# Kernel optimization log

Measured on AMD Instinct MI355X. Metric: run time of the kernel, lower is better.

## Reference

```python
import jax, jax.numpy as jnp
import numpy as np


def _ste(q, x):
    # straight-through estimator: forward = q, gradient = identity w.r.t. x
    return x + jax.lax.stop_gradient(q - x)


def quant_w(w, bit_w=8):
    # symmetric per-tensor weight quantization fused into QConv2d
    qmax = 2.0 ** (bit_w - 1) - 1.0
    scale = jnp.max(jnp.abs(w)) / qmax
    q = jnp.clip(jnp.round(w / scale), -qmax, qmax) * scale
    return _ste(q, w)


def quant_a(x, bit_a=8):
    # unsigned activation quantizer: clamp to [0,1], uniform bit_a levels
    n = 2.0 ** bit_a - 1.0
    xc = jnp.clip(x, 0.0, 1.0)
    q = jnp.round(xc * n) / n
    return _ste(q, xc)


def exp_norm2d(x, gamma, beta, eps=1e-5):
    # instance-style norm: per (N, C) statistics over spatial dims, affine
    mean = jnp.mean(x, axis=(2, 3), keepdims=True)
    var = jnp.var(x, axis=(2, 3), keepdims=True)
    xn = (x - mean) * jax.lax.rsqrt(var + eps)
    return xn * gamma[None, :, None, None] + beta[None, :, None, None]


def qconv(x, w, stride, pad, bit_w=8):
    wq = quant_w(w, bit_w)
    return jax.lax.conv_general_dilated(
        x, wq, window_strides=(stride, stride),
        padding=[(pad, pad), (pad, pad)],
        dimension_numbers=('NCHW', 'OIHW', 'NCHW'))


def setup_inputs() -> dict:
    key = jax.random.key(0)
    ks = jax.random.split(key, 4)
    C_in, C_out, H = 256, 512, 56
    return {
        'x': jax.random.normal(ks[0], (32, C_in, H, H), jnp.float32),
        'w1': jax.random.normal(ks[1], (C_out, C_in, 3, 3), jnp.float32) * 0.05,
        'g1': jnp.ones((C_out,), jnp.float32),
        'b1': jnp.zeros((C_out,), jnp.float32),
        'w2': jax.random.normal(ks[2], (C_out, C_out, 3, 3), jnp.float32) * 0.05,
        'g2': jnp.ones((C_out,), jnp.float32),
        'b2': jnp.zeros((C_out,), jnp.float32),
        'wp': jax.random.normal(ks[3], (C_out, C_in, 1, 1), jnp.float32) * 0.05,
        'gp': jnp.ones((C_out,), jnp.float32),
        'bp': jnp.zeros((C_out,), jnp.float32),
    }


def reference(x, w1, g1, b1, w2, g2, b2, wp, gp, bp):
    # main branch: QConv(s2) -> ExpNorm -> act quant -> QConv(s1) -> ExpNorm
    h = qconv(x, w1, stride=2, pad=1)
    h = exp_norm2d(h, g1, b1)
    h = quant_a(h, bit_a=8)
    h = qconv(h, w2, stride=1, pad=1)
    h = exp_norm2d(h, g2, b2)
    # projection shortcut: QConv 1x1 stride 2 -> ExpNorm
    s = qconv(x, wp, stride=2, pad=0)
    s = exp_norm2d(s, gp, bp)
    return h + s
```

## Files before the change

kernel.cpp:

```cpp
#include <hip/hip_runtime.h>
#include <cstdint>
#include <cstddef>


typedef unsigned short ushort_t;
typedef __attribute__((ext_vector_type(8))) short bf16x8;
typedef __attribute__((ext_vector_type(4))) int i32x4;

#define NB   32
#define C_IN 256
#define HIN  56
#define CO   512
#define OHW  784
#define OWD  28
#define MTOT (NB * OHW)

#define S_X  (6.0f / 127.0f)

constexpr size_t OFF_XH   = 0;
constexpr size_t OFF_A1   = OFF_XH  + 25690112;
constexpr size_t OFF_H2   = OFF_A1  + 12845056;
constexpr size_t OFF_S    = OFF_H2  + 25690112;
constexpr size_t OFF_WT1  = OFF_S   + 25690112;
constexpr size_t OFF_WT2  = OFF_WT1 + 1179648;
constexpr size_t OFF_WTP  = OFF_WT2 + 2359296;
constexpr size_t OFF_A1N  = OFF_WTP + 131072;
constexpr size_t OFF_B1N  = OFF_A1N + 65536;
constexpr size_t OFF_A2N  = OFF_B1N + 65536;
constexpr size_t OFF_B2N  = OFF_A2N + 65536;
constexpr size_t OFF_APN  = OFF_B2N + 65536;
constexpr size_t OFF_BPN  = OFF_APN + 65536;
constexpr size_t OFF_MX   = OFF_BPN + 65536;
constexpr size_t OFF_ZB   = OFF_MX  + 16;
constexpr size_t OFF_CS   = OFF_ZB  + 2048;
constexpr size_t OFF_PSUM = OFF_CS  + 18432;
constexpr size_t ZERO_LEN = 16 + 2048 + 18432 + 393216;

__device__ __forceinline__ ushort_t f2bf(float f) {
    unsigned u = __float_as_uint(f);
    u += 0x7FFFu + ((u >> 16) & 1u);
    return (ushort_t)(u >> 16);
}
__device__ __forceinline__ float bf2f(ushort_t u) {
    return __uint_as_float(((unsigned)u) << 16);
}

__device__ __forceinline__ void async_copy16(const void* g, const void* l) {
    auto gp = (const __attribute__((address_space(1))) unsigned int*)(uintptr_t)g;
    auto lp = (__attribute__((address_space(3))) unsigned int*)(unsigned int)(uintptr_t)l;
    __builtin_amdgcn_global_load_lds(gp, lp, 16, 0, 0);
}

__global__ void to_nhwc_i8_k(const float* __restrict__ x, signed char* __restrict__ xh) {
    __shared__ float tile[64][33];
    const int wt0 = blockIdx.x * 32;
    const int ct0 = blockIdx.y * 64;
    const int nh  = blockIdx.z;
    const int n = nh / HIN, h = nh - n * HIN;
    {
        const int tx = threadIdx.x & 31;
        const int ty = threadIdx.x >> 5;
        const int w  = wt0 + tx;
#pragma unroll
        for (int j = 0; j < 8; ++j) {
            int cl = ty + j * 8;
            if (w < HIN)
                tile[cl][tx] = x[(((size_t)n * C_IN + ct0 + cl) * HIN + h) * HIN + w];
        }
    }
    __syncthreads();
    {
        const float inv = 127.0f / 6.0f;
        const int tc4 = threadIdx.x & 15;
        const int tw  = threadIdx.x >> 4;
#pragma unroll
        for (int j = 0; j < 2; ++j) {
            int wl = tw + j * 16;
            int w  = wt0 + wl;
            if (w < HIN) {
                unsigned pk = 0;
#pragma unroll
                for (int k = 0; k < 4; ++k) {
                    float v = tile[tc4 * 4 + k][wl];
                    float q = fminf(127.f, fmaxf(-127.f, rintf(v * inv)));
                    pk |= ((unsigned)((int)q & 0xFF)) << (8 * k);
                }
                *(unsigned*)&xh[(((size_t)n * HIN + h) * HIN + w) * C_IN + ct0 + tc4 * 4] = pk;
            }
        }
    }
}

__global__ void absmax3_k(const float* __restrict__ w1, int n1,
                          const float* __restrict__ w2, int n2,
                          const float* __restrict__ wp, int np,
                          unsigned* out) {
    const float4* w; int nelem;
    if (blockIdx.y == 0)      { w = (const float4*)w1; nelem = n1 >> 2; }
    else if (blockIdx.y == 1) { w = (const float4*)w2; nelem = n2 >> 2; }
    else                      { w = (const float4*)wp; nelem = np >> 2; }
    int stride = gridDim.x * blockDim.x;
    float m = 0.f;
    for (int i = blockIdx.x * blockDim.x + threadIdx.x; i < nelem; i += stride) {
        float4 v = w[i];
        m = fmaxf(m, fmaxf(fmaxf(fabsf(v.x), fabsf(v.y)),
                           fmaxf(fabsf(v.z), fabsf(v.w))));
    }
#pragma unroll
    for (int off = 32; off > 0; off >>= 1)
        m = fmaxf(m, __shfl_down(m, off));
    if ((threadIdx.x & 63) == 0) atomicMax(out + blockIdx.y, __float_as_uint(m));
}

__global__ void quantw_all_k(const float* __restrict__ w1,
                             const float* __restrict__ w2,
                             const float* __restrict__ wp,
                             const unsigned* __restrict__ mx,
                             signed char* __restrict__ wt1,
                             signed char* __restrict__ wt2,
                             signed char* __restrict__ wtp,
                             float* __restrict__ cs) {
    const int b = blockIdx.x;
    if (b < 4608) {
        int idx = b * 256 + threadIdx.x;
        float scale = __uint_as_float(mx[0]) * (1.0f / 127.0f);
        float inv   = scale > 0.f ? 1.0f / scale : 0.f;
        int khw = idx / (CO * C_IN);
        int r   = idx - khw * (CO * C_IN);
        int co  = r / C_IN;
        int ci  = r - co * C_IN;
        float v  = w1[((size_t)co * C_IN + ci) * 9 + khw];
        float qv = rintf(v * inv);
        qv = fminf(127.f, fmaxf(-127.f, qv));
        wt1[idx] = (signed char)(int)qv;
    } else if (b < 13824) {
        int idx = (b - 4608) * 256 + threadIdx.x;
        float scale = __uint_as_float(mx[1]) * (1.0f / 127.0f);
        float inv   = scale > 0.f ? 1.0f / scale : 0.f;
        int khw = idx / (CO * CO);
        int r   = idx - khw * (CO * CO);
        int co  = r / CO;
        int ci  = r - co * CO;
        float v  = w2[((size_t)co * CO + ci) * 9 + khw];
        float qv = rintf(v * inv);
        qv = fminf(127.f, fmaxf(-127.f, qv));
        int iq = (int)qv;
        wt2[idx] = (signed char)iq;
        int s = iq;
#pragma unroll
        for (int off = 32; off > 0; off >>= 1)
            s += __shfl_down(s, off);
        if ((threadIdx.x & 63) == 0) atomicAdd(&cs[khw * CO + co], (float)s);
    } else {
        int idx = (b - 13824) * 256 + threadIdx.x;
        float scale = __uint_as_float(mx[2]) * (1.0f / 127.0f);
        float inv   = scale > 0.f ? 1.0f / scale : 0.f;
        int co  = idx / C_IN;
        int ci  = idx - co * C_IN;
        float v  = wp[(size_t)co * C_IN + ci];
        float qv = rintf(v * inv);
        qv = fminf(127.f, fmaxf(-127.f, qv));
        wtp[idx] = (signed char)(int)qv;
    }
}

template <int CIN, int KH, int KW, int STRIDE, int PAD, int IH, int IW, bool OFFSET>
__launch_bounds__(1024, 4)
__global__ void conv_i8_t(const signed char* __restrict__ xin,
                          const signed char* __restrict__ wt,
                          const float* __restrict__ colsum,
                          const unsigned* __restrict__ mxw,
                          float sxa,
                          ushort_t* __restrict__ out,
                          const signed char* __restrict__ zbuf,
                          float* __restrict__ psum, float* __restrict__ pss) {
    constexpr int BK   = 64;
    constexpr int CKT  = CIN / BK;
    constexpr int KT   = KH * KW * CKT;
    constexpr int NPER = KT / 2;

    __shared__ alignas(16) signed char As[4 * 256 * BK];
    __shared__ alignas(16) signed char Bs[4 * 256 * BK];

    const int tid  = threadIdx.x;
    const int lane = tid & 63;
    const int wv   = tid >> 6;
    const int wm   = wv >> 2;
    const int wn   = wv & 3;
    const int lrow = lane & 15;
    const int lq   = lane >> 4;

    const int bid = blockIdx.x;
    const int xcd = bid & 7;
    const int j   = bid >> 3;
    const int wg  = (xcd < 4 ? xcd * 25 : 100 + (xcd - 4) * 24) + j;
    const int m0  = (wg >> 1) * 256;
    const int co0 = (wg & 1) * 256;

    const int arow = tid >> 2;
    const int ach  = tid & 3;
    int abase; unsigned amask; int bco;
    {
        int m   = m0 + arow;
        int n   = m / OHW;
        int sp  = m - n * OHW;
        int oh  = sp / OWD, ow = sp - oh * OWD;
        int ihb = oh * STRIDE - PAD, iwb = ow * STRIDE - PAD;
        int swz = (ach ^ ((arow >> 1) & 3)) * 16;
        abase = (n * (IH * IW) + ihb * IW + iwb) * CIN + swz;
        unsigned mk = 0;
#pragma unroll
        for (int kh = 0; kh < KH; ++kh)
#pragma unroll
            for (int kw = 0; kw < KW; ++kw) {
                int ih = ihb + kh, iw = iwb + kw;
                if ((unsigned)ih < (unsigned)IH && (unsigned)iw < (unsigned)IW)
                    mk |= 1u << (kh * KW + kw);
            }
        amask = mk;
        bco = (co0 + arow) * CIN + swz;
    }

    auto stageA = [&](int buf, int aoff, int khw) {
        const signed char* src = ((amask >> khw) & 1)
            ? xin + (abase + aoff) : zbuf;
        async_copy16(src, (const void*)&As[buf * 16384 + wv * 1024]);
    };
    auto stageB = [&](int buf, int boff) {
        async_copy16(wt + (boff + bco), (const void*)&Bs[buf * 16384 + wv * 1024]);
    };

    i32x4 acc[4][4];
#pragma unroll
    for (int a = 0; a < 4; ++a)
#pragma unroll
        for (int b = 0; b < 4; ++b) acc[a][b] = {0, 0, 0, 0};

    stageB(0, 0);  stageA(0, 0, 0);
    stageB(1, BK); stageA(1, BK, 0);
    asm volatile("s_waitcnt vmcnt(0)" ::: "memory");
    __builtin_amdgcn_s_barrier();

    int khw_n = 0, kw_n = 0, ck_n = 2;
    int aoff_n = 2 * BK;
    int boff_n = 2 * BK;

#pragma unroll 1
    for (int p = 0; p < NPER; ++p) {
        const int t0 = 2 * p;
        if (p + 1 < NPER) {
#pragma unroll
            for (int u = 0; u < 2; ++u) {
                const int buf = (t0 + 2 + u) & 3;
                stageB(buf, boff_n);
                stageA(buf, aoff_n, khw_n);
                ck_n++;
                if (ck_n == CKT) {
                    ck_n = 0; khw_n++; kw_n++;
                    if (kw_n == KW) { kw_n = 0; aoff_n += (IW - KW) * CIN + BK; }
                    else            { aoff_n += BK; }
                    boff_n += (CO - 1) * CIN + BK;
                } else {
                    aoff_n += BK; boff_n += BK;
                }
            }
        }
        __builtin_amdgcn_sched_barrier(0);

#pragma unroll
        for (int sub = 0; sub < 2; ++sub) {
            const signed char* Acur = &As[((t0 + sub) & 3) * 16384];
            const signed char* Bcur = &Bs[((t0 + sub) & 3) * 16384];
            i32x4 af[4], bfr[4];
#pragma unroll
            for (int mi = 0; mi < 4; ++mi) {
                const int row = wm * 64 + mi * 16 + lrow;
                af[mi] = *(const i32x4*)&Acur[row * BK + ((lq ^ ((row >> 1) & 3)) * 16)];
            }
#pragma unroll
            for (int ni = 0; ni < 4; ++ni) {
                const int row = wn * 64 + ni * 16 + lrow;
                bfr[ni] = *(const i32x4*)&Bcur[row * BK + ((lq ^ ((row >> 1) & 3)) * 16)];
            }
#pragma unroll
            for (int mi = 0; mi < 4; ++mi)
#pragma unroll
                for (int ni = 0; ni < 4; ++ni)
                    acc[mi][ni] = __builtin_amdgcn_mfma_i32_16x16x64_i8(
                        af[mi], bfr[ni], acc[mi][ni], 0, 0, 0);
        }

        asm volatile("s_waitcnt vmcnt(0)" ::: "memory");
        __builtin_amdgcn_sched_barrier(0);
        __builtin_amdgcn_s_barrier();
    }

    const int mb = m0 + wm * 64 + lq * 4;
    const int cb = co0 + wn * 64 + lrow;
    const float sw = __uint_as_float(*mxw) * (1.0f / 127.0f);
    float sc, c128 = 0.f;
    if constexpr (OFFSET) { sc = sw * (1.0f / 255.0f); c128 = 128.0f * sc; }
    else                  { sc = sxa * sw; }

    float Sall[4], Sr0[4], Sr2[4], Sc0[4], Sc2[4], K0[4], K2[4], K6[4], K8[4];
    if constexpr (OFFSET) {
#pragma unroll
        for (int ni = 0; ni < 4; ++ni) {
            float cs9[9];
#pragma unroll
            for (int k = 0; k < 9; ++k) cs9[k] = colsum[k * CO + cb + ni * 16];
            Sall[ni] = cs9[0]+cs9[1]+cs9[2]+cs9[3]+cs9[4]+cs9[5]+cs9[6]+cs9[7]+cs9[8];
            Sr0[ni] = cs9[0]+cs9[1]+cs9[2];  Sr2[ni] = cs9[6]+cs9[7]+cs9[8];
            Sc0[ni] = cs9[0]+cs9[3]+cs9[6];  Sc2[ni] = cs9[2]+cs9[5]+cs9[8];
            K0[ni] = cs9[0]; K2[ni] = cs9[2]; K6[ni] = cs9[6]; K8[ni] = cs9[8];
        }
    }

    const int n0 = m0 / OHW;
    const int mS = (n0 + 1) * OHW;
    float sv[2][4], qvv[2][4];
#pragma unroll
    for (int g = 0; g < 2; ++g)
#pragma unroll
        for (int ni = 0; ni < 4; ++ni) { sv[g][ni] = 0.f; qvv[g][ni] = 0.f; }

#pragma unroll
    for (int mi = 0; mi < 4; ++mi)
#pragma unroll
        for (int r = 0; r < 4; ++r) {
            const int m  = mb + mi * 16 + r;
            const int n  = m / OHW;
            const int sp = m - n * OHW;
            const int oh = sp / OWD, ow = sp - oh * OWD;
            const int g  = (m >= mS) ? 1 : 0;
#pragma unroll
            for (int ni = 0; ni < 4; ++ni) {
                float val;
                if constexpr (OFFSET) {
                    float T = Sall[ni];
                    if (oh == 0)       T -= Sr0[ni];
                    if (oh == OWD - 1) T -= Sr2[ni];
                    if (ow == 0)       T -= Sc0[ni];
                    if (ow == OWD - 1) T -= Sc2[ni];
                    if (oh == 0 && ow == 0)             T += K0[ni];
                    if (oh == 0 && ow == OWD - 1)       T += K2[ni];
                    if (oh == OWD - 1 && ow == 0)       T += K6[ni];
                    if (oh == OWD - 1 && ow == OWD - 1) T += K8[ni];
                    val = sc * (float)acc[mi][ni][r] + c128 * T;
                } else {
                    val = sc * (float)acc[mi][ni][r];
                }
                out[(size_t)m * CO + (cb + ni * 16)] = f2bf(val);
                sv[g][ni] += val; qvv[g][ni] += val * val;
            }
        }
#pragma unroll
    for (int d = 16; d <= 32; d <<= 1)
#pragma unroll
        for (int g = 0; g < 2; ++g)
#pragma unroll
            for (int ni = 0; ni < 4; ++ni) {
                sv[g][ni]  += __shfl_xor(sv[g][ni], d);
                qvv[g][ni] += __shfl_xor(qvv[g][ni], d);
            }
    if (lq == 0) {
        const bool split = (mS < m0 + 256);
#pragma unroll
        for (int ni = 0; ni < 4; ++ni) {
            atomicAdd(&psum[n0 * CO + cb + ni * 16], sv[0][ni]);
            atomicAdd(&pss [n0 * CO + cb + ni * 16], qvv[0][ni]);
            if (split) {
                atomicAdd(&psum[(n0 + 1) * CO + cb + ni * 16], sv[1][ni]);
                atomicAdd(&pss [(n0 + 1) * CO + cb + ni * 16], qvv[1][ni]);
            }
        }
    }
}

__global__ void statsf3_k(const float* __restrict__ ps0, const float* __restrict__ qs0,
                          const float* __restrict__ g0, const float* __restrict__ bb0,
                          float* __restrict__ ao0, float* __restrict__ bo0,
                          const float* __restrict__ ps1, const float* __restrict__ qs1,
                          const float* __restrict__ g1, const float* __restrict__ bb1,
                          float* __restrict__ ao1, float* __restrict__ bo1,
                          const float* __restrict__ ps2, const float* __restrict__ qs2,
                          const float* __restrict__ g2, const float* __restrict__ bb2,
                          float* __restrict__ ao2, float* __restrict__ bo2) {
    const float *ps, *qs, *g, *bb; float *ao, *bo;
    if (blockIdx.y == 0)      { ps = ps0; qs = qs0; g = g0; bb = bb0; ao = ao0; bo = bo0; }
    else if (blockIdx.y == 1) { ps = ps1; qs = qs1; g = g1; bb = bb1; ao = ao1; bo = bo1; }
    else                      { ps = ps2; qs = qs2; g = g2; bb = bb2; ao = ao2; bo = bo2; }
    int idx = blockIdx.x * 256 + threadIdx.x;
    int c = idx & 511;
    float s  = ps[idx];
    float ss = qs[idx];
    float mean = s * (1.0f / 784.0f);
    float var  = ss * (1.0f / 784.0f) - mean * mean;
    float rstd = rsqrtf(var + 1e-5f);
    float a = rstd * g[c];
    ao[idx] = a;
    bo[idx] = bb[c] - mean * a;
}

__global__ void norm_quant_i8_k(const ushort_t* __restrict__ h, const float* __restrict__ a_,
                                const float* __restrict__ b_, signed char* __restrict__ o) {
    int idx = blockIdx.x * 256 + threadIdx.x;
    int row = idx >> 6;
    int c0  = (idx & 63) * 8;
    int n   = row / OHW;
    bf16x8 v = ((const bf16x8*)h)[idx];
    const float* ap = a_ + n * CO + c0;
    const float* bp = b_ + n * CO + c0;
    unsigned lo = 0, hi = 0;
#pragma unroll
    for (int k = 0; k < 8; ++k) {
        float f = bf2f((ushort_t)v[k]) * ap[k] + bp[k];
        float kq = rintf(fminf(fmaxf(f, 0.f), 1.f) * 255.f);
        int s8 = (int)kq - 128;
        unsigned b = (unsigned)(s8 & 0xFF);
        if (k < 4) lo |= b << (8 * k);
        else       hi |= b << (8 * (k - 4));
    }
    ((uint2*)o)[idx] = make_uint2(lo, hi);
}

__global__ void final_k(const ushort_t* __restrict__ h2, const ushort_t* __restrict__ s,
                        const float* __restrict__ a2, const float* __restrict__ b2,
                        const float* __restrict__ ap_, const float* __restrict__ bp_,
                        float* __restrict__ out) {
    __shared__ float tile[64][33];
    const int sp0 = blockIdx.x * 32;
    const int c0  = blockIdx.y * 64;
    const int n   = blockIdx.z;
    const int tx  = threadIdx.x & 31;
    const int ty  = threadIdx.x >> 5;
#pragma unroll
    for (int j = 0; j < 4; ++j) {
        int spl = ty + j * 8;
        int sp  = sp0 + spl;
        if (sp < OHW) {
            int c = c0 + tx * 2;
            size_t ix = ((size_t)n * OHW + sp) * CO + c;
            int ci = n * CO + c;
            ushort2 vh = *(const ushort2*)&h2[ix];
            ushort2 vs = *(const ushort2*)&s[ix];
            tile[tx * 2][spl] =
                bf2f(vh.x) * a2[ci] + b2[ci] + bf2f(vs.x) * ap_[ci] + bp_[ci];
            tile[tx * 2 + 1][spl] =
                bf2f(vh.y) * a2[ci + 1] + b2[ci + 1] + bf2f(vs.y) * ap_[ci + 1] + bp_[ci + 1];
        }
    }
    __syncthreads();
    const int sp = sp0 + tx;
#pragma unroll
    for (int j = 0; j < 8; ++j) {
        int cl = ty + j * 8;
        if (sp < OHW)
            out[((size_t)n * CO + c0 + cl) * OHW + sp] = tile[cl][tx];
    }
}

extern "C" void kernel_launch(void* const* d_in, const int* in_sizes, int n_in,
                              void* d_out, int out_size, void* d_ws, size_t ws_size,
                              hipStream_t stream) {
    const float* x  = (const float*)d_in[0];
    const float* w1 = (const float*)d_in[1];
    const float* g1 = (const float*)d_in[2];
    const float* b1 = (const float*)d_in[3];
    const float* w2 = (const float*)d_in[4];
    const float* g2 = (const float*)d_in[5];
    const float* b2 = (const float*)d_in[6];
    const float* wp = (const float*)d_in[7];
    const float* gp = (const float*)d_in[8];
    const float* bp = (const float*)d_in[9];
    float* out = (float*)d_out;
    char* ws = (char*)d_ws;

    signed char* xh    = (signed char*)(ws + OFF_XH);
    signed char* a1    = (signed char*)(ws + OFF_A1);
    ushort_t*    h2    = (ushort_t*)(ws + OFF_H2);
    ushort_t*    sbuf  = (ushort_t*)(ws + OFF_S);
    signed char* wt1i  = (signed char*)(ws + OFF_WT1);
    signed char* wt2i  = (signed char*)(ws + OFF_WT2);
    signed char* wtpi  = (signed char*)(ws + OFF_WTP);
    float*    a1n  = (float*)(ws + OFF_A1N);
    float*    b1n  = (float*)(ws + OFF_B1N);
    float*    a2n  = (float*)(ws + OFF_A2N);
    float*    b2n  = (float*)(ws + OFF_B2N);
    float*    apn  = (float*)(ws + OFF_APN);
    float*    bpn  = (float*)(ws + OFF_BPN);
    unsigned* mx   = (unsigned*)(ws + OFF_MX);
    signed char* zb = (signed char*)(ws + OFF_ZB);
    float*    cs   = (float*)(ws + OFF_CS);
    float*    psum1 = (float*)(ws + OFF_PSUM);
    float*    pss1  = (float*)(ws + OFF_PSUM + 65536);
    float*    psum2 = (float*)(ws + OFF_PSUM + 131072);
    float*    pss2  = (float*)(ws + OFF_PSUM + 196608);
    float*    psump = (float*)(ws + OFF_PSUM + 262144);
    float*    pssp  = (float*)(ws + OFF_PSUM + 327680);
    ushort_t* h1   = (ushort_t*)out;

    hipMemsetAsync(ws + OFF_MX, 0, ZERO_LEN, stream);

    to_nhwc_i8_k<<<dim3(2, 4, NB * HIN), 256, 0, stream>>>(x, xh);
    absmax3_k<<<dim3(512, 3), 256, 0, stream>>>(w1, CO * C_IN * 9,
                                                w2, CO * CO * 9,
                                                wp, C_IN * CO, mx);
    quantw_all_k<<<dim3(14336), 256, 0, stream>>>(w1, w2, wp, mx,
                                                  wt1i, wt2i, wtpi, cs);

    conv_i8_t<C_IN, 3, 3, 2, 1, HIN, HIN, false>
        <<<dim3(196), 1024, 0, stream>>>(xh, wt1i, cs, mx + 0, S_X, h1, zb,
                                         psum1, pss1);
    statsf3_k<<<dim3(64, 1), 256, 0, stream>>>(psum1, pss1, g1, b1, a1n, b1n,
                                               psum1, pss1, g1, b1, a1n, b1n,
                                               psum1, pss1, g1, b1, a1n, b1n);
    norm_quant_i8_k<<<dim3(MTOT * CO / 8 / 256), 256, 0, stream>>>(h1, a1n, b1n, a1);

    conv_i8_t<CO, 3, 3, 1, 1, 28, 28, true>
        <<<dim3(196), 1024, 0, stream>>>(a1, wt2i, cs, mx + 1, 1.0f, h2, zb,
                                         psum2, pss2);
    conv_i8_t<C_IN, 1, 1, 2, 0, HIN, HIN, false>
        <<<dim3(196), 1024, 0, stream>>>(xh, wtpi, cs, mx + 2, S_X, sbuf, zb,
                                         psump, pssp);

    statsf3_k<<<dim3(64, 2), 256, 0, stream>>>(psum2, pss2, g2, b2, a2n, b2n,
                                               psump, pssp, gp, bp, apn, bpn,
                                               psum2, pss2, g2, b2, a2n, b2n);

    final_k<<<dim3(25, 8, NB), 256, 0, stream>>>(h2, sbuf, a2n, b2n, apn, bpn, out);
}
```

Measured before the change: 277.4 us.

## Pre-swizzle weights into MFMA fragment layout and load B directly from global

Weight quantization now writes int8 weights in a per-k-tile, per-16-row fragment layout matching the MFMA operand order. The conv kernel drops the B shared-memory buffers and async B staging, and each lane loads its B fragments straight from global (L2-resident) memory at the start of each iteration. This halves LDS use and removes LDS traffic for B. The cost is global-load latency exposed in the inner loop, since B is no longer prefetched ahead, and redundant B loads across the wm warps.

```diff
diff --git a/kernel.cpp b/kernel.cpp
--- a/kernel.cpp
+++ b/kernel.cpp
@@ -49,6 +49,11 @@
     auto gp = (const __attribute__((address_space(1))) unsigned int*)(uintptr_t)g;
     auto lp = (__attribute__((address_space(3))) unsigned int*)(unsigned int)(uintptr_t)l;
     __builtin_amdgcn_global_load_lds(gp, lp, 16, 0, 0);
+}
+
+__device__ __forceinline__ size_t wfrag_addr(int kt, int co, int ci) {
+    return (size_t)kt * 32768 + (size_t)(co >> 4) * 1024 +
+           (size_t)(((co & 15) | (((ci >> 4) & 3) << 4)) * 16 + (ci & 15));
 }
 
 __global__ void to_nhwc_i8_k(const float* __restrict__ x, signed char* __restrict__ xh) {
@@ -132,7 +137,7 @@
         float v  = w1[((size_t)co * C_IN + ci) * 9 + khw];
         float qv = rintf(v * inv);
         qv = fminf(127.f, fmaxf(-127.f, qv));
-        wt1[idx] = (signed char)(int)qv;
+        wt1[wfrag_addr(khw * 4 + (ci >> 6), co, ci)] = (signed char)(int)qv;
     } else if (b < 13824) {
         int idx = (b - 4608) * 256 + threadIdx.x;
         float scale = __uint_as_float(mx[1]) * (1.0f / 127.0f);
@@ -145,7 +150,7 @@
         float qv = rintf(v * inv);
         qv = fminf(127.f, fmaxf(-127.f, qv));
         int iq = (int)qv;
-        wt2[idx] = (signed char)iq;
+        wt2[wfrag_addr(khw * 8 + (ci >> 6), co, ci)] = (signed char)iq;
         int s = iq;
 #pragma unroll
         for (int off = 32; off > 0; off >>= 1)
@@ -160,7 +165,7 @@
         float v  = wp[(size_t)co * C_IN + ci];
         float qv = rintf(v * inv);
         qv = fminf(127.f, fmaxf(-127.f, qv));
-        wtp[idx] = (signed char)(int)qv;
+        wtp[wfrag_addr(ci >> 6, co, ci)] = (signed char)(int)qv;
     }
 }
 
@@ -180,7 +185,6 @@
     constexpr int NPER = KT / 2;
 
     __shared__ alignas(16) signed char As[4 * 256 * BK];
-    __shared__ alignas(16) signed char Bs[4 * 256 * BK];
 
     const int tid  = threadIdx.x;
     const int lane = tid & 63;
@@ -199,7 +203,7 @@
 
     const int arow = tid >> 2;
     const int ach  = tid & 3;
-    int abase; unsigned amask; int bco;
+    int abase; unsigned amask;
     {
         int m   = m0 + arow;
         int n   = m / OHW;
@@ -218,7 +222,6 @@
                     mk |= 1u << (kh * KW + kw);
             }
         amask = mk;
-        bco = (co0 + arow) * CIN + swz;
     }
 
     auto stageA = [&](int buf, int aoff, int khw) {
@@ -226,9 +229,11 @@
             ? xin + (abase + aoff) : zbuf;
         async_copy16(src, (const void*)&As[buf * 16384 + wv * 1024]);
     };
-    auto stageB = [&](int buf, int boff) {
-        async_copy16(wt + (boff + bco), (const void*)&Bs[buf * 16384 + wv * 1024]);
-    };
+
+    size_t bbase[4];
+#pragma unroll
+    for (int ni = 0; ni < 4; ++ni)
+        bbase[ni] = (size_t)((co0 >> 4) + wn * 4 + ni) * 1024 + (size_t)lane * 16;
 
     i32x4 acc[4][4];
 #pragma unroll
@@ -236,32 +241,37 @@
 #pragma unroll
         for (int b = 0; b < 4; ++b) acc[a][b] = {0, 0, 0, 0};
 
-    stageB(0, 0);  stageA(0, 0, 0);
-    stageB(1, BK); stageA(1, BK, 0);
+    stageA(0, 0, 0);
+    stageA(1, BK, 0);
     asm volatile("s_waitcnt vmcnt(0)" ::: "memory");
     __builtin_amdgcn_s_barrier();
 
     int khw_n = 0, kw_n = 0, ck_n = 2;
     int aoff_n = 2 * BK;
-    int boff_n = 2 * BK;
 
 #pragma unroll 1
     for (int p = 0; p < NPER; ++p) {
         const int t0 = 2 * p;
+
+        i32x4 bfr[2][4];
+#pragma unroll
+        for (int sub = 0; sub < 2; ++sub)
+#pragma unroll
+            for (int ni = 0; ni < 4; ++ni)
+                bfr[sub][ni] = *(const i32x4*)(wt + (size_t)(t0 + sub) * 32768 + bbase[ni]);
+
         if (p + 1 < NPER) {
 #pragma unroll
             for (int u = 0; u < 2; ++u) {
                 const int buf = (t0 + 2 + u) & 3;
-                stageB(buf, boff_n);
                 stageA(buf, aoff_n, khw_n);
                 ck_n++;
                 if (ck_n == CKT) {
                     ck_n = 0; khw_n++; kw_n++;
                     if (kw_n == KW) { kw_n = 0; aoff_n += (IW - KW) * CIN + BK; }
                     else            { aoff_n += BK; }
-                    boff_n += (CO - 1) * CIN + BK;
                 } else {
-                    aoff_n += BK; boff_n += BK;
+                    aoff_n += BK;
                 }
             }
         }
@@ -270,24 +280,18 @@
 #pragma unroll
         for (int sub = 0; sub < 2; ++sub) {
             const signed char* Acur = &As[((t0 + sub) & 3) * 16384];
-            const signed char* Bcur = &Bs[((t0 + sub) & 3) * 16384];
-            i32x4 af[4], bfr[4];
+            i32x4 af[4];
 #pragma unroll
             for (int mi = 0; mi < 4; ++mi) {
                 const int row = wm * 64 + mi * 16 + lrow;
                 af[mi] = *(const i32x4*)&Acur[row * BK + ((lq ^ ((row >> 1) & 3)) * 16)];
             }
 #pragma unroll
-            for (int ni = 0; ni < 4; ++ni) {
-                const int row = wn * 64 + ni * 16 + lrow;
-                bfr[ni] = *(const i32x4*)&Bcur[row * BK + ((lq ^ ((row >> 1) & 3)) * 16)];
-            }
-#pragma unroll
             for (int mi = 0; mi < 4; ++mi)
 #pragma unroll
                 for (int ni = 0; ni < 4; ++ni)
                     acc[mi][ni] = __builtin_amdgcn_mfma_i32_16x16x64_i8(
-                        af[mi], bfr[ni], acc[mi][ni], 0, 0, 0);
+                        af[mi], bfr[sub][ni], acc[mi][ni], 0, 0, 0);
         }
 
         asm volatile("s_waitcnt vmcnt(0)" ::: "memory");
```

Result: slower. 303.2 us (+9.3%).
